# Kernel tuning notes

Hardware: AMD Instinct MI355X
Metric: run time of the kernel (lower is better)

Reference implementation:

```python
import jax, jax.numpy as jnp
import numpy as np

B, T, S, H = 8, 512, 512, 128


def setup_inputs() -> dict:
    key = jax.random.key(0)
    ks = jax.random.split(key, 8)
    query = jax.random.normal(ks[0], (B, T, H), dtype=jnp.float32)
    encoder_outputs = jax.random.normal(ks[1], (B, S, H), dtype=jnp.float32)
    src_lengths = jax.random.randint(ks[2], (B,), 1, S + 1)
    src_lengths = src_lengths.at[0].set(S)  # torch mask width == lengths.max() must equal S
    scale = 1.0 / np.sqrt(H)
    W_h = jax.random.normal(ks[3], (H, H), dtype=jnp.float32) * scale
    W_s = jax.random.normal(ks[4], (H, H), dtype=jnp.float32) * scale
    v = jax.random.normal(ks[5], (H,), dtype=jnp.float32) * scale
    W_out_w = jax.random.normal(ks[6], (H, 2 * H), dtype=jnp.float32) * (1.0 / np.sqrt(2 * H))
    W_out_b = jax.random.normal(ks[7], (H,), dtype=jnp.float32) * 0.01
    return {"query": query, "encoder_outputs": encoder_outputs,
            "src_lengths": src_lengths, "W_h": W_h, "W_s": W_s, "v": v,
            "W_out_w": W_out_w, "W_out_b": W_out_b}


def reference(query, encoder_outputs, src_lengths, W_h, W_s, v, W_out_w, W_out_b):
    # query: (B,T,H); encoder_outputs: (B,S,H)
    S_ = encoder_outputs.shape[1]
    WS = jnp.einsum('bth,oh->bto', query, W_s)            # (B,T,H)
    WH = jnp.einsum('bsh,oh->bso', encoder_outputs, W_h)  # (B,S,H)
    # additive scores: v^T tanh(W_s s_t + W_h h_i)  -> (B,T,S)
    scores = jnp.einsum('btsh,h->bts', jnp.tanh(WS[:, :, None, :] + WH[:, None, :, :]), v)
    mask = jnp.arange(S_) < src_lengths[:, None]          # (B,S)
    # faithful quirk: original zeroes (not -inf) masked scores before softmax
    scores = jnp.where(mask[:, None, :], scores, 0.0)
    attn = jax.nn.softmax(scores, axis=-1)                # (B,T,S)
    ct = jnp.einsum('bts,bsh->bth', attn, encoder_outputs)
    concat = jnp.concatenate([ct, query], axis=-1)        # (B,T,2H)
    return jnp.tanh(jnp.einsum('btc,oc->bto', concat, W_out_w) + W_out_b)
```

## Files before the change

kernel.cpp:

```cpp
#include <hip/hip_runtime.h>

#define NB 8
#define NT 512
#define NS 512
#define NH 128
#define C2LOG2E 2.8853900817779268f

__device__ __forceinline__ float fast_exp2(float x) { return __builtin_amdgcn_exp2f(x); }
__device__ __forceinline__ float fast_rcp(float x)  { return __builtin_amdgcn_rcpf(x); }
__device__ __forceinline__ float fast_tanh(float x) {
  float e = fast_exp2(x * C2LOG2E);
  return 1.0f - 2.0f * fast_rcp(e + 1.0f);
}

__device__ __forceinline__ float dot4(float4 a, float4 b) {
  return (a.x * b.x + a.y * b.y) + (a.z * b.z + a.w * b.w);
}

__device__ __forceinline__ float2 quad_acc2(float4 e, float4 vv,
                                            float2 F0, float2 F1,
                                            float2 F2, float2 F3, float2 acc) {
  float P0x = fmaf(e.x, F0.x, 1.f), P0y = fmaf(e.x, F0.y, 1.f);
  float P1x = fmaf(e.y, F1.x, 1.f), P1y = fmaf(e.y, F1.y, 1.f);
  float P2x = fmaf(e.z, F2.x, 1.f), P2y = fmaf(e.z, F2.y, 1.f);
  float P3x = fmaf(e.w, F3.x, 1.f), P3y = fmaf(e.w, F3.y, 1.f);
  float d01x = P0x * P1x, d01y = P0y * P1y;
  float d23x = P2x * P3x, d23y = P2y * P3y;
  float n01x = fmaf(vv.x, P1x, vv.y * P0x);
  float n01y = fmaf(vv.x, P1y, vv.y * P0y);
  float n23x = fmaf(vv.z, P3x, vv.w * P2x);
  float n23y = fmaf(vv.z, P3y, vv.w * P2y);
  float numx = fmaf(n01x, d23x, n23x * d01x);
  float numy = fmaf(n01y, d23y, n23y * d01y);
  acc.x = fmaf(numx, fast_rcp(d01x * d23x), acc.x);
  acc.y = fmaf(numy, fast_rcp(d01y * d23y), acc.y);
  return acc;
}

__global__ __launch_bounds__(256) void bah_proj_kernel(
    const float* __restrict__ query, const float* __restrict__ enc,
    const float* __restrict__ W_s, const float* __restrict__ W_h,
    const float* __restrict__ Wout, const float* __restrict__ Woutb,
    float* __restrict__ EWS, float* __restrict__ EWHT,
    float* __restrict__ ENCW, float* __restrict__ QW2) {
  __shared__ __align__(16) float lds_w[64 * 132];
  __shared__ __align__(16) float lds_x[32 * 132];
  const int set = blockIdx.x >> 8;
  const int blk = blockIdx.x & 255;
  const int rb = blk >> 1, ch = blk & 1;
  const int r0 = rb * 32, c0 = ch * 64;
  const int tid = threadIdx.x;
  const float* in = (set == 1 || set == 2) ? enc : query;
  const float* Wb; int wst;
  if (set == 0)      { Wb = W_s;        wst = 128; }
  else if (set == 1) { Wb = W_h;        wst = 128; }
  else if (set == 2) { Wb = Wout;       wst = 256; }
  else               { Wb = Wout + 128; wst = 256; }
  for (int i = tid; i < 2048; i += 256) {
    int r = i >> 5, c4 = i & 31;
    *(float4*)(lds_w + r * 132 + c4 * 4) =
        *(const float4*)(Wb + (c0 + r) * wst + c4 * 4);
  }
  for (int i = tid; i < 1024; i += 256) {
    int r = i >> 5, c4 = i & 31;
    *(float4*)(lds_x + r * 132 + c4 * 4) =
        *(const float4*)(in + (r0 + r) * NH + c4 * 4);
  }
  __syncthreads();
  const int cg = tid & 31;
  const int rg = tid >> 5;
  float acc[4][2] = {{0,0},{0,0},{0,0},{0,0}};
  for (int k4 = 0; k4 < 32; ++k4) {
    float4 xa[4], wb[2];
    #pragma unroll
    for (int i = 0; i < 4; ++i)
      xa[i] = *(const float4*)(lds_x + (rg * 4 + i) * 132 + k4 * 4);
    #pragma unroll
    for (int m = 0; m < 2; ++m)
      wb[m] = *(const float4*)(lds_w + (cg + 32 * m) * 132 + k4 * 4);
    #pragma unroll
    for (int i = 0; i < 4; ++i)
      #pragma unroll
      for (int m = 0; m < 2; ++m)
        acc[i][m] += dot4(xa[i], wb[m]);
  }
  if (set == 0) {
    #pragma unroll
    for (int i = 0; i < 4; ++i)
      #pragma unroll
      for (int m = 0; m < 2; ++m)
        EWS[(r0 + rg * 4 + i) * NH + c0 + cg + 32 * m] =
            fast_exp2(C2LOG2E * acc[i][m]);
  } else if (set == 1) {
    __syncthreads();
    #pragma unroll
    for (int i = 0; i < 4; ++i)
      #pragma unroll
      for (int m = 0; m < 2; ++m)
        lds_x[(cg + 32 * m) * 33 + rg * 4 + i] = fast_exp2(C2LOG2E * acc[i][m]);
    __syncthreads();
    const int b = r0 >> 9, sl0 = r0 & 511;
    const int s_lane = tid & 31, hr = tid >> 5;
    #pragma unroll
    for (int j = 0; j < 8; ++j)
      EWHT[b * NH * NS + (c0 + hr * 8 + j) * NS + sl0 + s_lane] =
          lds_x[(hr * 8 + j) * 33 + s_lane];
  } else if (set == 2) {
    #pragma unroll
    for (int i = 0; i < 4; ++i)
      #pragma unroll
      for (int m = 0; m < 2; ++m)
        ENCW[(r0 + rg * 4 + i) * NH + c0 + cg + 32 * m] = acc[i][m];
  } else {
    #pragma unroll
    for (int i = 0; i < 4; ++i)
      #pragma unroll
      for (int m = 0; m < 2; ++m) {
        int c = c0 + cg + 32 * m;
        QW2[(r0 + rg * 4 + i) * NH + c] = acc[i][m] + Woutb[c];
      }
  }
}

__global__ __launch_bounds__(512) void bah_mega_kernel(
    const float* __restrict__ EWS, const float* __restrict__ EWHT,
    const float* __restrict__ v, const float* __restrict__ ENCW,
    const float* __restrict__ QW2, const int* __restrict__ src_len,
    float* __restrict__ out) {
  __shared__ __align__(16) float smem[13824];
  float* s_v   = smem;
  float* s_et  = smem + 128;
  float* s_aT  = smem + 1184;
  float* s_par = smem + 5280;
  float* s_sc  = smem + 9632;
  float* s_red = smem + 13760;

  const int tid = threadIdx.x;
  const int bb = blockIdx.x >> 6;
  const int t0 = (blockIdx.x & 63) * 8;
  const int len = src_len[bb];

  if (tid < 32) *(float4*)(s_v + tid * 4) = *(const float4*)(v + tid * 4);
  if (tid < 256) {
    int r = tid >> 5, c4 = tid & 31;
    *(float4*)(s_et + r * 132 + c4 * 4) =
        *(const float4*)(EWS + (bb * NT + t0 + r) * NH + c4 * 4);
  }
  __syncthreads();

  float V0;
  {
    float2 vv = *(const float2*)(s_v + (tid & 63) * 2);
    V0 = vv.x + vv.y;
    #pragma unroll
    for (int msk = 1; msk <= 32; msk <<= 1)
      V0 += __shfl_xor(V0, msk, 64);
  }

  const int tg = tid >> 8, sp = tid & 255;
  const int sbase = sp * 2;
  const int h0 = tg * 64;
  float2 acc2[8];
  #pragma unroll
  for (int i = 0; i < 8; ++i) { acc2[i].x = 0.f; acc2[i].y = 0.f; }
  const int wave_s0 = (sp & ~63) * 2;
  if (wave_s0 < len) {
    const float* fb = EWHT + bb * NH * NS + h0 * NS + sbase;
    for (int ho = 0; ho < 8; ++ho) {
      const float* fh = fb + ho * 8 * NS;
      float2 F0 = *(const float2*)(fh + 0 * NS);
      float2 F1 = *(const float2*)(fh + 1 * NS);
      float2 F2 = *(const float2*)(fh + 2 * NS);
      float2 F3 = *(const float2*)(fh + 3 * NS);
      float2 F4 = *(const float2*)(fh + 4 * NS);
      float2 F5 = *(const float2*)(fh + 5 * NS);
      float2 F6 = *(const float2*)(fh + 6 * NS);
      float2 F7 = *(const float2*)(fh + 7 * NS);
      float4 va = *(const float4*)(s_v + h0 + ho * 8);
      float4 vb = *(const float4*)(s_v + h0 + ho * 8 + 4);
      #pragma unroll
      for (int tt = 0; tt < 8; ++tt) {
        float4 e0 = *(const float4*)(s_et + tt * 132 + h0 + ho * 8);
        float4 e1 = *(const float4*)(s_et + tt * 132 + h0 + ho * 8 + 4);
        acc2[tt] = quad_acc2(e0, va, F0, F1, F2, F3, acc2[tt]);
        acc2[tt] = quad_acc2(e1, vb, F4, F5, F6, F7, acc2[tt]);
      }
    }
  }
  if (tg == 1) {
    #pragma unroll
    for (int tt = 0; tt < 8; ++tt)
      *(float2*)(s_par + sp * 17 + tt * 2) = acc2[tt];
  }
  __syncthreads();
  if (tg == 0) {
    #pragma unroll
    for (int tt = 0; tt < 8; ++tt) {
      float2 oth = *(const float2*)(s_par + sp * 17 + tt * 2);
      float sx = acc2[tt].x + oth.x;
      float sy = acc2[tt].y + oth.y;
      float2 r;
      r.x = (sbase + 0 < len) ? fmaf(-2.f, sx, V0) : 0.f;
      r.y = (sbase + 1 < len) ? fmaf(-2.f, sy, V0) : 0.f;
      *(float2*)(s_sc + tt * 516 + sbase) = r;
    }
  }
  __syncthreads();

  const int t = tid & 7;
  const int c = tid >> 3;
  const int wv = tid >> 6;
  float pv[8];
  float mx = -3.4e38f;
  #pragma unroll
  for (int k = 0; k < 8; ++k) {
    pv[k] = s_sc[t * 516 + c + 64 * k];
    mx = fmaxf(mx, pv[k]);
  }
  #pragma unroll
  for (int msk = 8; msk <= 32; msk <<= 1)
    mx = fmaxf(mx, __shfl_xor(mx, msk, 64));
  if ((tid & 63) < 8) s_red[wv * 8 + t] = mx;
  __syncthreads();
  #pragma unroll
  for (int j = 1; j < 8; ++j) mx = fmaxf(mx, s_red[j * 8 + t]);
  mx = fmaxf(mx, s_red[t]);
  __syncthreads();
  float sum = 0.f;
  #pragma unroll
  for (int k = 0; k < 8; ++k) {
    pv[k] = fast_exp2((pv[k] - mx) * 1.4426950408889634f);
    sum += pv[k];
  }
  #pragma unroll
  for (int msk = 8; msk <= 32; msk <<= 1)
    sum += __shfl_xor(sum, msk, 64);
  if ((tid & 63) < 8) s_red[wv * 8 + t] = sum;
  __syncthreads();
  sum = 0.f;
  #pragma unroll
  for (int j = 0; j < 8; ++j) sum += s_red[j * 8 + t];
  const float rd = fast_rcp(sum);
  #pragma unroll
  for (int k = 0; k < 8; ++k)
    s_aT[(c + 64 * k) * 8 + t] = pv[k] * rd;
  __syncthreads();

  const int hg = tid & 31, sg = tid >> 5;
  float4 a8[8] = {{0,0,0,0},{0,0,0,0},{0,0,0,0},{0,0,0,0},
                  {0,0,0,0},{0,0,0,0},{0,0,0,0},{0,0,0,0}};
  float4 Tc = {0.f, 0.f, 0.f, 0.f};
  const float* eb = ENCW + bb * NS * NH + hg * 4;
  for (int k = 0; k < 32; ++k) {
    int s = sg * 32 + k;
    float4 e  = *(const float4*)(eb + s * NH);
    if (s < len) {
      float4 w0 = *(const float4*)(s_aT + s * 8);
      float4 w1 = *(const float4*)(s_aT + s * 8 + 4);
      a8[0].x += w0.x*e.x; a8[0].y += w0.x*e.y; a8[0].z += w0.x*e.z; a8[0].w += w0.x*e.w;
      a8[1].x += w0.y*e.x; a8[1].y += w0.y*e.y; a8[1].z += w0.y*e.z; a8[1].w += w0.y*e.w;
      a8[2].x += w0.z*e.x; a8[2].y += w0.z*e.y; a8[2].z += w0.z*e.z; a8[2].w += w0.z*e.w;
      a8[3].x += w0.w*e.x; a8[3].y += w0.w*e.y; a8[3].z += w0.w*e.z; a8[3].w += w0.w*e.w;
      a8[4].x += w1.x*e.x; a8[4].y += w1.x*e.y; a8[4].z += w1.x*e.z; a8[4].w += w1.x*e.w;
      a8[5].x += w1.y*e.x; a8[5].y += w1.y*e.y; a8[5].z += w1.y*e.z; a8[5].w += w1.y*e.w;
      a8[6].x += w1.z*e.x; a8[6].y += w1.z*e.y; a8[6].z += w1.z*e.z; a8[6].w += w1.z*e.w;
      a8[7].x += w1.w*e.x; a8[7].y += w1.w*e.y; a8[7].z += w1.w*e.z; a8[7].w += w1.w*e.w;
    } else {
      Tc.x += e.x; Tc.y += e.y; Tc.z += e.z; Tc.w += e.w;
    }
  }
  if (len < NS) {
    float4 w0 = *(const float4*)(s_aT + len * 8);
    float4 w1 = *(const float4*)(s_aT + len * 8 + 4);
    a8[0].x += w0.x*Tc.x; a8[0].y += w0.x*Tc.y; a8[0].z += w0.x*Tc.z; a8[0].w += w0.x*Tc.w;
    a8[1].x += w0.y*Tc.x; a8[1].y += w0.y*Tc.y; a8[1].z += w0.y*Tc.z; a8[1].w += w0.y*Tc.w;
    a8[2].x += w0.z*Tc.x; a8[2].y += w0.z*Tc.y; a8[2].z += w0.z*Tc.z; a8[2].w += w0.z*Tc.w;
    a8[3].x += w0.w*Tc.x; a8[3].y += w0.w*Tc.y; a8[3].z += w0.w*Tc.z; a8[3].w += w0.w*Tc.w;
    a8[4].x += w1.x*Tc.x; a8[4].y += w1.x*Tc.y; a8[4].z += w1.x*Tc.z; a8[4].w += w1.x*Tc.w;
    a8[5].x += w1.y*Tc.x; a8[5].y += w1.y*Tc.y; a8[5].z += w1.y*Tc.z; a8[5].w += w1.y*Tc.w;
    a8[6].x += w1.z*Tc.x; a8[6].y += w1.z*Tc.y; a8[6].z += w1.z*Tc.z; a8[6].w += w1.z*Tc.w;
    a8[7].x += w1.w*Tc.x; a8[7].y += w1.w*Tc.y; a8[7].z += w1.w*Tc.z; a8[7].w += w1.w*Tc.w;
  }
  #pragma unroll
  for (int i = 0; i < 8; ++i) {
    a8[i].x += __shfl_xor(a8[i].x, 32, 64);
    a8[i].y += __shfl_xor(a8[i].y, 32, 64);
    a8[i].z += __shfl_xor(a8[i].z, 32, 64);
    a8[i].w += __shfl_xor(a8[i].w, 32, 64);
  }
  float* lred = s_par;
  if ((tid & 63) < 32) {
    #pragma unroll
    for (int i = 0; i < 8; ++i)
      *(float4*)(lred + wv * 1024 + i * 128 + hg * 4) = a8[i];
  }
  __syncthreads();
  if (tid < 256) {
    int tt = tid >> 5, hh = tid & 31;
    float4 o = {0.f, 0.f, 0.f, 0.f};
    #pragma unroll
    for (int j = 0; j < 8; ++j) {
      float4 p = *(const float4*)(lred + j * 1024 + tt * 128 + hh * 4);
      o.x += p.x; o.y += p.y; o.z += p.z; o.w += p.w;
    }
    const int row = bb * NT + t0 + tt;
    float4 q4 = *(const float4*)(QW2 + row * NH + hh * 4);
    float4 r;
    r.x = fast_tanh(o.x + q4.x);
    r.y = fast_tanh(o.y + q4.y);
    r.z = fast_tanh(o.z + q4.z);
    r.w = fast_tanh(o.w + q4.w);
    *(float4*)(out + row * NH + hh * 4) = r;
  }
}

extern "C" void kernel_launch(void* const* d_in, const int* in_sizes, int n_in,
                              void* d_out, int out_size, void* d_ws, size_t ws_size,
                              hipStream_t stream) {
  const float* query = (const float*)d_in[0];
  const float* enc   = (const float*)d_in[1];
  const int*   slen  = (const int*)d_in[2];
  const float* W_h   = (const float*)d_in[3];
  const float* W_s   = (const float*)d_in[4];
  const float* v     = (const float*)d_in[5];
  const float* Woutw = (const float*)d_in[6];
  const float* Woutb = (const float*)d_in[7];
  float* out = (float*)d_out;

  float* ws = (float*)d_ws;
  float* EWS  = ws;
  float* EWHT = ws + 524288;
  float* ENCW = ws + 1048576;
  float* QW2  = ws + 1572864;

  bah_proj_kernel<<<1024, 256, 0, stream>>>(query, enc, W_s, W_h, Woutw,
                                            Woutb, EWS, EWHT, ENCW, QW2);
  bah_mega_kernel<<<512, 512, 0, stream>>>(EWS, EWHT, v, ENCW, QW2, slen, out);
}
```

Measured before the change: 122.1 us.

## Interleave block-to-batch mapping, software-prefetch loads, and remove masked-tail branch in context loop

Remaps block indices in both kernels so neighbouring blocks cover different batches and row tiles, aiming to spread memory traffic and balance work across compute units given the variable source lengths. Adds register double-buffering of the EWHT tiles in the score loop and of the encoder rows in the context loop, so the next loads are issued before the current FMA work. The context loop loses its per-step length branch and the separate tail-sum correction, and always multiplies by the stored attention weights. This relies on s_aT already holding the right weights for masked positions, and double-buffering raises register pressure.

Measured after the change: 122.9 us. Within noise of the previous version (+0.6%).

```diff
diff --git a/kernel.cpp b/kernel.cpp
--- a/kernel.cpp
+++ b/kernel.cpp
@@ -46,7 +46,8 @@
   __shared__ __align__(16) float lds_w[64 * 132];
   __shared__ __align__(16) float lds_x[32 * 132];
   const int set = blockIdx.x >> 8;
-  const int blk = blockIdx.x & 255;
+  const int u   = blockIdx.x & 255;
+  const int blk = ((u & 7) << 5) | (u >> 3);
   const int rb = blk >> 1, ch = blk & 1;
   const int r0 = rb * 32, c0 = ch * 64;
   const int tid = threadIdx.x;
@@ -136,8 +137,8 @@
   float* s_red = smem + 13760;
 
   const int tid = threadIdx.x;
-  const int bb = blockIdx.x >> 6;
-  const int t0 = (blockIdx.x & 63) * 8;
+  const int bb = blockIdx.x & 7;
+  const int t0 = (blockIdx.x >> 3) * 8;
   const int len = src_len[bb];
 
   if (tid < 32) *(float4*)(s_v + tid * 4) = *(const float4*)(v + tid * 4);
@@ -166,25 +167,27 @@
   const int wave_s0 = (sp & ~63) * 2;
   if (wave_s0 < len) {
     const float* fb = EWHT + bb * NH * NS + h0 * NS + sbase;
+    float2 F[8];
+    #pragma unroll
+    for (int j = 0; j < 8; ++j) F[j] = *(const float2*)(fb + j * NS);
     for (int ho = 0; ho < 8; ++ho) {
-      const float* fh = fb + ho * 8 * NS;
-      float2 F0 = *(const float2*)(fh + 0 * NS);
-      float2 F1 = *(const float2*)(fh + 1 * NS);
-      float2 F2 = *(const float2*)(fh + 2 * NS);
-      float2 F3 = *(const float2*)(fh + 3 * NS);
-      float2 F4 = *(const float2*)(fh + 4 * NS);
-      float2 F5 = *(const float2*)(fh + 5 * NS);
-      float2 F6 = *(const float2*)(fh + 6 * NS);
-      float2 F7 = *(const float2*)(fh + 7 * NS);
+      float2 Fn[8];
+      if (ho < 7) {
+        const float* fh = fb + (ho + 1) * 8 * NS;
+        #pragma unroll
+        for (int j = 0; j < 8; ++j) Fn[j] = *(const float2*)(fh + j * NS);
+      }
       float4 va = *(const float4*)(s_v + h0 + ho * 8);
       float4 vb = *(const float4*)(s_v + h0 + ho * 8 + 4);
       #pragma unroll
       for (int tt = 0; tt < 8; ++tt) {
         float4 e0 = *(const float4*)(s_et + tt * 132 + h0 + ho * 8);
         float4 e1 = *(const float4*)(s_et + tt * 132 + h0 + ho * 8 + 4);
-        acc2[tt] = quad_acc2(e0, va, F0, F1, F2, F3, acc2[tt]);
-        acc2[tt] = quad_acc2(e1, vb, F4, F5, F6, F7, acc2[tt]);
+        acc2[tt] = quad_acc2(e0, va, F[0], F[1], F[2], F[3], acc2[tt]);
+        acc2[tt] = quad_acc2(e1, vb, F[4], F[5], F[6], F[7], acc2[tt]);
       }
+      #pragma unroll
+      for (int j = 0; j < 8; ++j) F[j] = Fn[j];
     }
   }
   if (tg == 1) {
@@ -249,37 +252,23 @@
   const int hg = tid & 31, sg = tid >> 5;
   float4 a8[8] = {{0,0,0,0},{0,0,0,0},{0,0,0,0},{0,0,0,0},
                   {0,0,0,0},{0,0,0,0},{0,0,0,0},{0,0,0,0}};
-  float4 Tc = {0.f, 0.f, 0.f, 0.f};
   const float* eb = ENCW + bb * NS * NH + hg * 4;
+  float4 e = *(const float4*)(eb + (sg * 32) * NH);
   for (int k = 0; k < 32; ++k) {
     int s = sg * 32 + k;
-    float4 e  = *(const float4*)(eb + s * NH);
-    if (s < len) {
-      float4 w0 = *(const float4*)(s_aT + s * 8);
-      float4 w1 = *(const float4*)(s_aT + s * 8 + 4);
-      a8[0].x += w0.x*e.x; a8[0].y += w0.x*e.y; a8[0].z += w0.x*e.z; a8[0].w += w0.x*e.w;
-      a8[1].x += w0.y*e.x; a8[1].y += w0.y*e.y; a8[1].z += w0.y*e.z; a8[1].w += w0.y*e.w;
-      a8[2].x += w0.z*e.x; a8[2].y += w0.z*e.y; a8[2].z += w0.z*e.z; a8[2].w += w0.z*e.w;
-      a8[3].x += w0.w*e.x; a8[3].y += w0.w*e.y; a8[3].z += w0.w*e.z; a8[3].w += w0.w*e.w;
-      a8[4].x += w1.x*e.x; a8[4].y += w1.x*e.y; a8[4].z += w1.x*e.z; a8[4].w += w1.x*e.w;
-      a8[5].x += w1.y*e.x; a8[5].y += w1.y*e.y; a8[5].z += w1.y*e.z; a8[5].w += w1.y*e.w;
-      a8[6].x += w1.z*e.x; a8[6].y += w1.z*e.y; a8[6].z += w1.z*e.z; a8[6].w += w1.z*e.w;
-      a8[7].x += w1.w*e.x; a8[7].y += w1.w*e.y; a8[7].z += w1.w*e.z; a8[7].w += w1.w*e.w;
-    } else {
-      Tc.x += e.x; Tc.y += e.y; Tc.z += e.z; Tc.w += e.w;
-    }
-  }
-  if (len < NS) {
-    float4 w0 = *(const float4*)(s_aT + len * 8);
-    float4 w1 = *(const float4*)(s_aT + len * 8 + 4);
-    a8[0].x += w0.x*Tc.x; a8[0].y += w0.x*Tc.y; a8[0].z += w0.x*Tc.z; a8[0].w += w0.x*Tc.w;
-    a8[1].x += w0.y*Tc.x; a8[1].y += w0.y*Tc.y; a8[1].z += w0.y*Tc.z; a8[1].w += w0.y*Tc.w;
-    a8[2].x += w0.z*Tc.x; a8[2].y += w0.z*Tc.y; a8[2].z += w0.z*Tc.z; a8[2].w += w0.z*Tc.w;
-    a8[3].x += w0.w*Tc.x; a8[3].y += w0.w*Tc.y; a8[3].z += w0.w*Tc.z; a8[3].w += w0.w*Tc.w;
-    a8[4].x += w1.x*Tc.x; a8[4].y += w1.x*Tc.y; a8[4].z += w1.x*Tc.z; a8[4].w += w1.x*Tc.w;
-    a8[5].x += w1.y*Tc.x; a8[5].y += w1.y*Tc.y; a8[5].z += w1.y*Tc.z; a8[5].w += w1.y*Tc.w;
-    a8[6].x += w1.z*Tc.x; a8[6].y += w1.z*Tc.y; a8[6].z += w1.z*Tc.z; a8[6].w += w1.z*Tc.w;
-    a8[7].x += w1.w*Tc.x; a8[7].y += w1.w*Tc.y; a8[7].z += w1.w*Tc.z; a8[7].w += w1.w*Tc.w;
+    float4 en = e;
+    if (k < 31) en = *(const float4*)(eb + (s + 1) * NH);
+    float4 w0 = *(const float4*)(s_aT + s * 8);
+    float4 w1 = *(const float4*)(s_aT + s * 8 + 4);
+    a8[0].x += w0.x*e.x; a8[0].y += w0.x*e.y; a8[0].z += w0.x*e.z; a8[0].w += w0.x*e.w;
+    a8[1].x += w0.y*e.x; a8[1].y += w0.y*e.y; a8[1].z += w0.y*e.z; a8[1].w += w0.y*e.w;
+    a8[2].x += w0.z*e.x; a8[2].y += w0.z*e.y; a8[2].z += w0.z*e.z; a8[2].w += w0.z*e.w;
+    a8[3].x += w0.w*e.x; a8[3].y += w0.w*e.y; a8[3].z += w0.w*e.z; a8[3].w += w0.w*e.w;
+    a8[4].x += w1.x*e.x; a8[4].y += w1.x*e.y; a8[4].z += w1.x*e.z; a8[4].w += w1.x*e.w;
+    a8[5].x += w1.y*e.x; a8[5].y += w1.y*e.y; a8[5].z += w1.y*e.z; a8[5].w += w1.y*e.w;
+    a8[6].x += w1.z*e.x; a8[6].y += w1.z*e.y; a8[6].z += w1.z*e.z; a8[6].w += w1.z*e.w;
+    a8[7].x += w1.w*e.x; a8[7].y += w1.w*e.y; a8[7].z += w1.w*e.z; a8[7].w += w1.w*e.w;
+    e = en;
   }
   #pragma unroll
   for (int i = 0; i < 8; ++i) {
```

## Shrink attention blocks to 4 query rows and 256 threads, drop h-split reduction

Applied to the files above, without the earlier changes.

The fused attention kernel now handles 4 query rows per block with 256 threads (1024 blocks) instead of 8 rows with 512 threads. Each thread walks all 128 hidden dims itself, so the cross-thread-group LDS reduction and one barrier go away. Shared memory drops sharply, which may allow more resident blocks. The context loop also loses its masked-tail shortcut and always reads all S encoder rows, relying on zeroed scores. The trade-off is that EWHT tiles are reloaded by twice as many blocks, and each block carries a longer serial loop.

Measured after the change: 118.0 us. 3.4% less time.

```diff
diff --git a/kernel.cpp b/kernel.cpp
--- a/kernel.cpp
+++ b/kernel.cpp
@@ -122,26 +122,25 @@
   }
 }
 
-__global__ __launch_bounds__(512) void bah_mega_kernel(
+__global__ __launch_bounds__(256) void bah_mega_kernel(
     const float* __restrict__ EWS, const float* __restrict__ EWHT,
     const float* __restrict__ v, const float* __restrict__ ENCW,
     const float* __restrict__ QW2, const int* __restrict__ src_len,
     float* __restrict__ out) {
-  __shared__ __align__(16) float smem[13824];
+  __shared__ __align__(16) float smem[4784];
   float* s_v   = smem;
   float* s_et  = smem + 128;
-  float* s_aT  = smem + 1184;
-  float* s_par = smem + 5280;
-  float* s_sc  = smem + 9632;
-  float* s_red = smem + 13760;
+  float* s_aT  = smem + 656;
+  float* s_sc  = smem + 2704;
+  float* s_red = smem + 4768;
 
   const int tid = threadIdx.x;
-  const int bb = blockIdx.x >> 6;
-  const int t0 = (blockIdx.x & 63) * 8;
+  const int bb = blockIdx.x >> 7;
+  const int t0 = (blockIdx.x & 127) * 4;
   const int len = src_len[bb];
 
   if (tid < 32) *(float4*)(s_v + tid * 4) = *(const float4*)(v + tid * 4);
-  if (tid < 256) {
+  if (tid < 128) {
     int r = tid >> 5, c4 = tid & 31;
     *(float4*)(s_et + r * 132 + c4 * 4) =
         *(const float4*)(EWS + (bb * NT + t0 + r) * NH + c4 * 4);
@@ -157,16 +156,15 @@
       V0 += __shfl_xor(V0, msk, 64);
   }
 
-  const int tg = tid >> 8, sp = tid & 255;
+  const int sp = tid;
   const int sbase = sp * 2;
-  const int h0 = tg * 64;
-  float2 acc2[8];
-  #pragma unroll
-  for (int i = 0; i < 8; ++i) { acc2[i].x = 0.f; acc2[i].y = 0.f; }
-  const int wave_s0 = (sp & ~63) * 2;
+  float2 acc2[4];
+  #pragma unroll
+  for (int i = 0; i < 4; ++i) { acc2[i].x = 0.f; acc2[i].y = 0.f; }
+  const int wave_s0 = (tid & ~63) * 2;
   if (wave_s0 < len) {
-    const float* fb = EWHT + bb * NH * NS + h0 * NS + sbase;
-    for (int ho = 0; ho < 8; ++ho) {
+    const float* fb = EWHT + bb * NH * NS + sbase;
+    for (int ho = 0; ho < 16; ++ho) {
       const float* fh = fb + ho * 8 * NS;
       float2 F0 = *(const float2*)(fh + 0 * NS);
       float2 F1 = *(const float2*)(fh + 1 * NS);
@@ -176,39 +174,28 @@
       float2 F5 = *(const float2*)(fh + 5 * NS);
       float2 F6 = *(const float2*)(fh + 6 * NS);
       float2 F7 = *(const float2*)(fh + 7 * NS);
-      float4 va = *(const float4*)(s_v + h0 + ho * 8);
-      float4 vb = *(const float4*)(s_v + h0 + ho * 8 + 4);
-      #pragma unroll
-      for (int tt = 0; tt < 8; ++tt) {
-        float4 e0 = *(const float4*)(s_et + tt * 132 + h0 + ho * 8);
-        float4 e1 = *(const float4*)(s_et + tt * 132 + h0 + ho * 8 + 4);
+      float4 va = *(const float4*)(s_v + ho * 8);
+      float4 vb = *(const float4*)(s_v + ho * 8 + 4);
+      #pragma unroll
+      for (int tt = 0; tt < 4; ++tt) {
+        float4 e0 = *(const float4*)(s_et + tt * 132 + ho * 8);
+        float4 e1 = *(const float4*)(s_et + tt * 132 + ho * 8 + 4);
         acc2[tt] = quad_acc2(e0, va, F0, F1, F2, F3, acc2[tt]);
         acc2[tt] = quad_acc2(e1, vb, F4, F5, F6, F7, acc2[tt]);
       }
     }
   }
-  if (tg == 1) {
-    #pragma unroll
-    for (int tt = 0; tt < 8; ++tt)
-      *(float2*)(s_par + sp * 17 + tt * 2) = acc2[tt];
-  }
-  __syncthreads();
-  if (tg == 0) {
-    #pragma unroll
-    for (int tt = 0; tt < 8; ++tt) {
-      float2 oth = *(const float2*)(s_par + sp * 17 + tt * 2);
-      float sx = acc2[tt].x + oth.x;
-      float sy = acc2[tt].y + oth.y;
-      float2 r;
-      r.x = (sbase + 0 < len) ? fmaf(-2.f, sx, V0) : 0.f;
-      r.y = (sbase + 1 < len) ? fmaf(-2.f, sy, V0) : 0.f;
-      *(float2*)(s_sc + tt * 516 + sbase) = r;
-    }
-  }
-  __syncthreads();
-
-  const int t = tid & 7;
-  const int c = tid >> 3;
+  #pragma unroll
+  for (int tt = 0; tt < 4; ++tt) {
+    float2 r;
+    r.x = (sbase + 0 < len) ? fmaf(-2.f, acc2[tt].x, V0) : 0.f;
+    r.y = (sbase + 1 < len) ? fmaf(-2.f, acc2[tt].y, V0) : 0.f;
+    *(float2*)(s_sc + tt * 516 + sbase) = r;
+  }
+  __syncthreads();
+
+  const int t = tid & 3;
+  const int c = tid >> 2;
   const int wv = tid >> 6;
   float pv[8];
   float mx = -3.4e38f;
@@ -218,13 +205,12 @@
     mx = fmaxf(mx, pv[k]);
   }
   #pragma unroll
-  for (int msk = 8; msk <= 32; msk <<= 1)
+  for (int msk = 4; msk <= 32; msk <<= 1)
     mx = fmaxf(mx, __shfl_xor(mx, msk, 64));
-  if ((tid & 63) < 8) s_red[wv * 8 + t] = mx;
-  __syncthreads();
-  #pragma unroll
-  for (int j = 1; j < 8; ++j) mx = fmaxf(mx, s_red[j * 8 + t]);
-  mx = fmaxf(mx, s_red[t]);
+  if ((tid & 63) < 4) s_red[wv * 4 + t] = mx;
+  __syncthreads();
+  #pragma unroll
+  for (int j = 0; j < 4; ++j) mx = fmaxf(mx, s_red[j * 4 + t]);
   __syncthreads();
   float sum = 0.f;
   #pragma unroll
@@ -233,84 +219,59 @@
     sum += pv[k];
   }
   #pragma unroll
-  for (int msk = 8; msk <= 32; msk <<= 1)
+  for (int msk = 4; msk <= 32; msk <<= 1)
     sum += __shfl_xor(sum, msk, 64);
-  if ((tid & 63) < 8) s_red[wv * 8 + t] = sum;
+  if ((tid & 63) < 4) s_red[wv * 4 + t] = sum;
   __syncthreads();
   sum = 0.f;
   #pragma unroll
-  for (int j = 0; j < 8; ++j) sum += s_red[j * 8 + t];
+  for (int j = 0; j < 4; ++j) sum += s_red[j * 4 + t];
   const float rd = fast_rcp(sum);
   #pragma unroll
   for (int k = 0; k < 8; ++k)
-    s_aT[(c + 64 * k) * 8 + t] = pv[k] * rd;
+    s_aT[(c + 64 * k) * 4 + t] = pv[k] * rd;
   __syncthreads();
 
   const int hg = tid & 31, sg = tid >> 5;
-  float4 a8[8] = {{0,0,0,0},{0,0,0,0},{0,0,0,0},{0,0,0,0},
-                  {0,0,0,0},{0,0,0,0},{0,0,0,0},{0,0,0,0}};
-  float4 Tc = {0.f, 0.f, 0.f, 0.f};
+  float4 a8[4] = {{0,0,0,0},{0,0,0,0},{0,0,0,0},{0,0,0,0}};
   const float* eb = ENCW + bb * NS * NH + hg * 4;
-  for (int k = 0; k < 32; ++k) {
-    int s = sg * 32 + k;
-    float4 e  = *(const float4*)(eb + s * NH);
-    if (s < len) {
-      float4 w0 = *(const float4*)(s_aT + s * 8);
-      float4 w1 = *(const float4*)(s_aT + s * 8 + 4);
-      a8[0].x += w0.x*e.x; a8[0].y += w0.x*e.y; a8[0].z += w0.x*e.z; a8[0].w += w0.x*e.w;
-      a8[1].x += w0.y*e.x; a8[1].y += w0.y*e.y; a8[1].z += w0.y*e.z; a8[1].w += w0.y*e.w;
-      a8[2].x += w0.z*e.x; a8[2].y += w0.z*e.y; a8[2].z += w0.z*e.z; a8[2].w += w0.z*e.w;
-      a8[3].x += w0.w*e.x; a8[3].y += w0.w*e.y; a8[3].z += w0.w*e.z; a8[3].w += w0.w*e.w;
-      a8[4].x += w1.x*e.x; a8[4].y += w1.x*e.y; a8[4].z += w1.x*e.z; a8[4].w += w1.x*e.w;
-      a8[5].x += w1.y*e.x; a8[5].y += w1.y*e.y; a8[5].z += w1.y*e.z; a8[5].w += w1.y*e.w;
-      a8[6].x += w1.z*e.x; a8[6].y += w1.z*e.y; a8[6].z += w1.z*e.z; a8[6].w += w1.z*e.w;
-      a8[7].x += w1.w*e.x; a8[7].y += w1.w*e.y; a8[7].z += w1.w*e.z; a8[7].w += w1.w*e.w;
-    } else {
-      Tc.x += e.x; Tc.y += e.y; Tc.z += e.z; Tc.w += e.w;
-    }
-  }
-  if (len < NS) {
-    float4 w0 = *(const float4*)(s_aT + len * 8);
-    float4 w1 = *(const float4*)(s_aT + len * 8 + 4);
-    a8[0].x += w0.x*Tc.x; a8[0].y += w0.x*Tc.y; a8[0].z += w0.x*Tc.z; a8[0].w += w0.x*Tc.w;
-    a8[1].x += w0.y*Tc.x; a8[1].y += w0.y*Tc.y; a8[1].z += w0.y*Tc.z; a8[1].w += w0.y*Tc.w;
-    a8[2].x += w0.z*Tc.x; a8[2].y += w0.z*Tc.y; a8[2].z += w0.z*Tc.z; a8[2].w += w0.z*Tc.w;
-    a8[3].x += w0.w*Tc.x; a8[3].y += w0.w*Tc.y; a8[3].z += w0.w*Tc.z; a8[3].w += w0.w*Tc.w;
-    a8[4].x += w1.x*Tc.x; a8[4].y += w1.x*Tc.y; a8[4].z += w1.x*Tc.z; a8[4].w += w1.x*Tc.w;
-    a8[5].x += w1.y*Tc.x; a8[5].y += w1.y*Tc.y; a8[5].z += w1.y*Tc.z; a8[5].w += w1.y*Tc.w;
-    a8[6].x += w1.z*Tc.x; a8[6].y += w1.z*Tc.y; a8[6].z += w1.z*Tc.z; a8[6].w += w1.z*Tc.w;
-    a8[7].x += w1.w*Tc.x; a8[7].y += w1.w*Tc.y; a8[7].z += w1.w*Tc.z; a8[7].w += w1.w*Tc.w;
-  }
-  #pragma unroll
-  for (int i = 0; i < 8; ++i) {
+  for (int k = 0; k < 64; ++k) {
+    int s = sg * 64 + k;
+    float4 e = *(const float4*)(eb + s * NH);
+    float4 w = *(const float4*)(s_aT + s * 4);
+    a8[0].x += w.x*e.x; a8[0].y += w.x*e.y; a8[0].z += w.x*e.z; a8[0].w += w.x*e.w;
+    a8[1].x += w.y*e.x; a8[1].y += w.y*e.y; a8[1].z += w.y*e.z; a8[1].w += w.y*e.w;
+    a8[2].x += w.z*e.x; a8[2].y += w.z*e.y; a8[2].z += w.z*e.z; a8[2].w += w.z*e.w;
+    a8[3].x += w.w*e.x; a8[3].y += w.w*e.y; a8[3].z += w.w*e.z; a8[3].w += w.w*e.w;
+  }
+  #pragma unroll
+  for (int i = 0; i < 4; ++i) {
     a8[i].x += __shfl_xor(a8[i].x, 32, 64);
     a8[i].y += __shfl_xor(a8[i].y, 32, 64);
     a8[i].z += __shfl_xor(a8[i].z, 32, 64);
     a8[i].w += __shfl_xor(a8[i].w, 32, 64);
   }
-  float* lred = s_par;
+  float* lred = s_sc;
   if ((tid & 63) < 32) {
     #pragma unroll
-    for (int i = 0; i < 8; ++i)
-      *(float4*)(lred + wv * 1024 + i * 128 + hg * 4) = a8[i];
-  }
-  __syncthreads();
-  if (tid < 256) {
-    int tt = tid >> 5, hh = tid & 31;
-    float4 o = {0.f, 0.f, 0.f, 0.f};
-    #pragma unroll
-    for (int j = 0; j < 8; ++j) {
-      float4 p = *(const float4*)(lred + j * 1024 + tt * 128 + hh * 4);
-      o.x += p.x; o.y += p.y; o.z += p.z; o.w += p.w;
+    for (int i = 0; i < 4; ++i)
+      *(float4*)(lred + wv * 512 + i * 128 + hg * 4) = a8[i];
+  }
+  __syncthreads();
+  {
+    int tt = tid >> 6, h2 = tid & 63;
+    float2 o = {0.f, 0.f};
+    #pragma unroll
+    for (int j = 0; j < 4; ++j) {
+      float2 p = *(const float2*)(lred + j * 512 + tt * 128 + h2 * 2);
+      o.x += p.x; o.y += p.y;
     }
     const int row = bb * NT + t0 + tt;
-    float4 q4 = *(const float4*)(QW2 + row * NH + hh * 4);
-    float4 r;
-    r.x = fast_tanh(o.x + q4.x);
-    r.y = fast_tanh(o.y + q4.y);
-    r.z = fast_tanh(o.z + q4.z);
-    r.w = fast_tanh(o.w + q4.w);
-    *(float4*)(out + row * NH + hh * 4) = r;
+    float2 q2 = *(const float2*)(QW2 + row * NH + h2 * 2);
+    float2 r;
+    r.x = fast_tanh(o.x + q2.x);
+    r.y = fast_tanh(o.y + q2.y);
+    *(float2*)(out + row * NH + h2 * 2) = r;
   }
 }
 
@@ -335,5 +296,5 @@
 
   bah_proj_kernel<<<1024, 256, 0, stream>>>(query, enc, W_s, W_h, Woutw,
                                             Woutb, EWS, EWHT, ENCW, QW2);
-  bah_mega_kernel<<<512, 512, 0, stream>>>(EWS, EWHT, v, ENCW, QW2, slen, out);
-}
+  bah_mega_kernel<<<1024, 256, 0, stream>>>(EWS, EWHT, v, ENCW, QW2, slen, out);
+}
```
